# Kernel tuning notes

Measured on AMD Instinct MI355X. Metric: run time of the kernel, lower is better.

The kernel has to match this reference:

```python
import jax, jax.numpy as jnp
import numpy as np

N = 50000   # nodes
DEG = 16    # avg degree
E = N * DEG # edges
D = 64      # 2*vl, vl=32
EPS = 1e-12 # F.normalize eps


def setup_inputs() -> dict:
    key = jax.random.key(0)
    k1, k2, k3, k4 = jax.random.split(key, 4)
    ft_lv0 = jax.random.normal(k1, (N, D), dtype=jnp.float32)
    # fc weights: Linear(4*vl, 2*vl, bias=False) -> shape [2*vl, 4*vl] = [64, 128]
    W1 = jax.random.normal(k2, (D, 2 * D), dtype=jnp.float32) * 0.05
    W2 = jax.random.normal(k3, (D, 2 * D), dtype=jnp.float32) * 0.05
    # edge list: tgt[e] gathers ft[nbr[e]] and sums into node tgt[e]
    nbr = jax.random.randint(k4, (E,), 0, N, dtype=jnp.int32)
    tgt = jnp.repeat(jnp.arange(N, dtype=jnp.int32), DEG)  # sorted segment ids
    return {"ft_lv0": ft_lv0, "W1": W1, "W2": W2, "nbr": nbr, "tgt": tgt}


def _gcn_layer(ft, W, nbr, tgt, n_nodes):
    # sum-pool neighbor features: pool[n] = sum_{m in adj(n)} ft[m]
    pool = jax.ops.segment_sum(ft[nbr], tgt, num_segments=n_nodes)  # [N, D]
    # concat(node + pool, node * pool); pool==0 for isolated nodes reproduces
    # the original else-branch cat(node, zeros) exactly.
    z = jnp.concatenate([ft + pool, ft * pool], axis=-1)  # [N, 2D]
    return jax.nn.relu(z @ W.T)  # [N, D]


def reference(ft_lv0, W1, W2, nbr, tgt):
    n_nodes = ft_lv0.shape[0]
    ft_lv1 = _gcn_layer(ft_lv0, W1, nbr, tgt, n_nodes)
    ft_lv2 = _gcn_layer(ft_lv1, W2, nbr, tgt, n_nodes)
    # F.normalize(z, dim=-1): z / max(||z||_2, eps)
    norm = jnp.linalg.norm(ft_lv2, axis=-1, keepdims=True)
    return ft_lv2 / jnp.maximum(norm, EPS)
```

## Files before the change

### kernel.cpp

```cpp
#include <hip/hip_runtime.h>
#include <hip/hip_bf16.h>


#define N_NODES 50000
#define DEG 16
#define DIM 64
#define NTILES 3125

typedef __attribute__((ext_vector_type(8))) short short8;
typedef __attribute__((ext_vector_type(8))) unsigned short ushort8;
typedef __attribute__((ext_vector_type(4))) float f32x4;

__device__ __forceinline__ unsigned short f2b(float f) {
  unsigned int u = __float_as_uint(f);
  u = (u + 0x7FFFu + ((u >> 16) & 1u)) >> 16;
  return (unsigned short)u;
}
#define LOF(u) __uint_as_float((u) << 16)
#define HIF(u) __uint_as_float((u) & 0xFFFF0000u)

__global__ void cast_bf16(const float* __restrict__ in, unsigned short* __restrict__ out, int n4) {
  const int i = blockIdx.x * 256 + threadIdx.x;
  if (i < n4) {
    const float4 v = reinterpret_cast<const float4*>(in)[i];
    ushort4 o4;
    o4.x = f2b(v.x); o4.y = f2b(v.y); o4.z = f2b(v.z); o4.w = f2b(v.w);
    reinterpret_cast<ushort4*>(out)[i] = o4;
  }
}

__global__ void prep_w(const float* __restrict__ W1, const float* __restrict__ W2,
                       unsigned short* __restrict__ Wb) {
  const int task = blockIdx.x * 256 + threadIdx.x;
  if (task >= 2048) return;
  const int which = task >> 10;
  const int f = (task >> 6) & 15;
  const int l = task & 63;
  const int ct = f >> 2, ks = f & 3;
  const int wn = l & 15, wg = l >> 4;
  const float* W = which ? W2 : W1;
  const float* wp = W + (ct * 16 + wn) * 128 + ks * 32 + wg * 8;
  const float4 w0 = *(const float4*)wp;
  const float4 w1 = *(const float4*)(wp + 4);
  ushort8 o;
  o[0] = f2b(w0.x); o[1] = f2b(w0.y); o[2] = f2b(w0.z); o[3] = f2b(w0.w);
  o[4] = f2b(w1.x); o[5] = f2b(w1.y); o[6] = f2b(w1.z); o[7] = f2b(w1.w);
  *(ushort8*)(Wb + ((size_t)(which * 16 + f) * 64 + l) * 8) = o;
}

#define GATHER_AND_STAGE_V3()                                                  \
  _Pragma("unroll 2")                                                          \
  for (int p = 0; p < 4; ++p) {                                                \
    const int pp = sub * 4 + p;                                                \
    const int rA = (base + 2 * pp) * DEG;                                      \
    const int4 ia0 = *(const int4*)(nbr + rA);                                 \
    const int4 ia1 = *(const int4*)(nbr + rA + 4);                             \
    const int4 ia2 = *(const int4*)(nbr + rA + 8);                             \
    const int4 ia3 = *(const int4*)(nbr + rA + 12);                            \
    const int4 ib0 = *(const int4*)(nbr + rA + 16);                            \
    const int4 ib1 = *(const int4*)(nbr + rA + 20);                            \
    const int4 ib2 = *(const int4*)(nbr + rA + 24);                            \
    const int4 ib3 = *(const int4*)(nbr + rA + 28);                            \
    const unsigned int un  = ftp[(base + 2 * pp + half) * 32 + c];             \
    const unsigned int v0  = ftp[(half ? ib0.x : ia0.x) * 32 + c];             \
    const unsigned int v1  = ftp[(half ? ib0.y : ia0.y) * 32 + c];             \
    const unsigned int v2  = ftp[(half ? ib0.z : ia0.z) * 32 + c];             \
    const unsigned int v3  = ftp[(half ? ib0.w : ia0.w) * 32 + c];             \
    const unsigned int v4  = ftp[(half ? ib1.x : ia1.x) * 32 + c];             \
    const unsigned int v5  = ftp[(half ? ib1.y : ia1.y) * 32 + c];             \
    const unsigned int v6  = ftp[(half ? ib1.z : ia1.z) * 32 + c];             \
    const unsigned int v7  = ftp[(half ? ib1.w : ia1.w) * 32 + c];             \
    const unsigned int v8  = ftp[(half ? ib2.x : ia2.x) * 32 + c];             \
    const unsigned int v9  = ftp[(half ? ib2.y : ia2.y) * 32 + c];             \
    const unsigned int v10 = ftp[(half ? ib2.z : ia2.z) * 32 + c];             \
    const unsigned int v11 = ftp[(half ? ib2.w : ia2.w) * 32 + c];             \
    const unsigned int v12 = ftp[(half ? ib3.x : ia3.x) * 32 + c];             \
    const unsigned int v13 = ftp[(half ? ib3.y : ia3.y) * 32 + c];             \
    const unsigned int v14 = ftp[(half ? ib3.z : ia3.z) * 32 + c];             \
    const unsigned int v15 = ftp[(half ? ib3.w : ia3.w) * 32 + c];             \
    const float plo = (((LOF(v0) + LOF(v1)) + (LOF(v2) + LOF(v3))) +           \
                       ((LOF(v4) + LOF(v5)) + (LOF(v6) + LOF(v7)))) +          \
                      (((LOF(v8) + LOF(v9)) + (LOF(v10) + LOF(v11))) +         \
                       ((LOF(v12) + LOF(v13)) + (LOF(v14) + LOF(v15))));       \
    const float phi = (((HIF(v0) + HIF(v1)) + (HIF(v2) + HIF(v3))) +           \
                       ((HIF(v4) + HIF(v5)) + (HIF(v6) + HIF(v7)))) +          \
                      (((HIF(v8) + HIF(v9)) + (HIF(v10) + HIF(v11))) +         \
                       ((HIF(v12) + HIF(v13)) + (HIF(v14) + HIF(v15))));       \
    const float nlo = LOF(un), nhi = HIF(un);                                  \
    const float z1lo = nlo + plo, z1hi = nhi + phi;                            \
    const float z2lo = nlo * plo, z2hi = nhi * phi;                            \
    unsigned int z1p, z2p;                                                     \
    asm("v_cvt_pk_bf16_f32 %0, %1, %2" : "=v"(z1p) : "v"(z1lo), "v"(z1hi));    \
    asm("v_cvt_pk_bf16_f32 %0, %1, %2" : "=v"(z2p) : "v"(z2lo), "v"(z2hi));    \
    const int r = 2 * pp + half;                                               \
    const int cs = c ^ ((r & 7) << 2);                                         \
    Azs[r * 64 + cs] = z1p;                                                    \
    Azs[r * 64 + 32 + cs] = z2p;                                               \
  }

#define PRELOAD_W()                                                            \
  short8 Bf[4][4];                                                             \
  {                                                                            \
    const short8* wf = (const short8*)Wb;                                      \
    _Pragma("unroll")                                                          \
    for (int f = 0; f < 16; ++f) Bf[f >> 2][f & 3] = wf[f * 64 + lane];        \
  }

#define MFMA_ACCUM()                                                           \
  f32x4 ac0 = {0.f, 0.f, 0.f, 0.f}, ac1 = ac0, ac2 = ac0, ac3 = ac0;          \
  {                                                                            \
    const int arow = lane & 15, agrp = lane >> 4;                              \
    const int axor = (arow & 7) << 2;                                          \
    _Pragma("unroll")                                                          \
    for (int ks = 0; ks < 4; ++ks) {                                           \
      const short8 a =                                                         \
          *(const short8*)&Azs[arow * 64 + ((ks * 16 + agrp * 4) ^ axor)];     \
      ac0 = __builtin_amdgcn_mfma_f32_16x16x32_bf16(a, Bf[0][ks], ac0, 0, 0, 0);\
      ac1 = __builtin_amdgcn_mfma_f32_16x16x32_bf16(a, Bf[1][ks], ac1, 0, 0, 0);\
      ac2 = __builtin_amdgcn_mfma_f32_16x16x32_bf16(a, Bf[2][ks], ac2, 0, 0, 0);\
      ac3 = __builtin_amdgcn_mfma_f32_16x16x32_bf16(a, Bf[3][ks], ac3, 0, 0, 0);\
    }                                                                          \
  }

__global__ __launch_bounds__(256, 4)
void gcn_mfma1(const unsigned short* __restrict__ ftb,
               const unsigned short* __restrict__ Wb,
               const int* __restrict__ nbr,
               unsigned short* __restrict__ outb) {
  __shared__ unsigned int Az[2][1024];
  const int tid = threadIdx.x;
  const int lane = tid & 63, wid = tid >> 6;
  const int tl = wid >> 1, sub = wid & 1;
  const int t = __builtin_amdgcn_readfirstlane(blockIdx.x * 2 + tl);
  const bool active = (t < NTILES);
  const int base = t * 16;
  const int half = lane >> 5, c = lane & 31;
  const unsigned int* ftp = (const unsigned int*)ftb;
  unsigned int* Azs = &Az[tl][0];

  if (active) { GATHER_AND_STAGE_V3(); }
  PRELOAD_W();
  __syncthreads();
  MFMA_ACCUM();
  __syncthreads();

  if (active) {
    unsigned short* sh = (unsigned short*)Azs;
    const int colf = lane & 15, rgrp = lane >> 4;
    if ((rgrp >> 1) == sub) {
#define STG1(AC, CT)                                                           \
      _Pragma("unroll")                                                        \
      for (int rr = 0; rr < 4; ++rr)                                           \
        sh[(rgrp * 4 + rr) * 64 + (((CT)*16 + colf) ^ (rgrp << 4))] =          \
            f2b(fmaxf(AC[rr], 0.f));
      STG1(ac0, 0) STG1(ac1, 1) STG1(ac2, 2) STG1(ac3, 3)
#undef STG1
    }
    const int row = sub * 8 + (lane >> 3), b = lane & 7;
    const int rg = row >> 2;
    const ushort8 d = *(const ushort8*)&sh[row * 64 + ((b ^ (rg << 1)) << 3)];
    *(ushort8*)(outb + (size_t)(base + row) * 64 + b * 8) = d;
  }
}

__global__ __launch_bounds__(256, 4)
void gcn_mfma2(const unsigned short* __restrict__ ftb,
               const unsigned short* __restrict__ Wb,
               const int* __restrict__ nbr,
               float* __restrict__ out) {
  __shared__ unsigned int Az[2][1024];
  const int tid = threadIdx.x;
  const int lane = tid & 63, wid = tid >> 6;
  const int tl = wid >> 1, sub = wid & 1;
  const int t = __builtin_amdgcn_readfirstlane(blockIdx.x * 2 + tl);
  const bool active = (t < NTILES);
  const int base = t * 16;
  const int half = lane >> 5, c = lane & 31;
  const unsigned int* ftp = (const unsigned int*)ftb;
  unsigned int* Azs = &Az[tl][0];

  if (active) { GATHER_AND_STAGE_V3(); }
  PRELOAD_W();
  __syncthreads();
  MFMA_ACCUM();
  __syncthreads();

  if (active) {
    float v0[4], v1[4], v2[4], v3[4];
#pragma unroll
    for (int rr = 0; rr < 4; ++rr) {
      v0[rr] = fmaxf(ac0[rr], 0.f);
      v1[rr] = fmaxf(ac1[rr], 0.f);
      v2[rr] = fmaxf(ac2[rr], 0.f);
      v3[rr] = fmaxf(ac3[rr], 0.f);
    }
    float s0 = v0[0]*v0[0] + v1[0]*v1[0] + v2[0]*v2[0] + v3[0]*v3[0];
    float s1 = v0[1]*v0[1] + v1[1]*v1[1] + v2[1]*v2[1] + v3[1]*v3[1];
    float s2 = v0[2]*v0[2] + v1[2]*v1[2] + v2[2]*v2[2] + v3[2]*v3[2];
    float s3 = v0[3]*v0[3] + v1[3]*v1[3] + v2[3]*v2[3] + v3[3]*v3[3];
#pragma unroll
    for (int w = 1; w < 16; w <<= 1) {
      s0 += __shfl_xor(s0, w, 64);
      s1 += __shfl_xor(s1, w, 64);
      s2 += __shfl_xor(s2, w, 64);
      s3 += __shfl_xor(s3, w, 64);
    }
    const float kk[4] = {1.f / fmaxf(sqrtf(s0), 1e-12f),
                         1.f / fmaxf(sqrtf(s1), 1e-12f),
                         1.f / fmaxf(sqrtf(s2), 1e-12f),
                         1.f / fmaxf(sqrtf(s3), 1e-12f)};

    float* shf = (float*)Azs;
    const int colf = lane & 15, rgrp = lane >> 4;
    if ((rgrp >> 1) == sub) {
#define STG2(VA, CT)                                                           \
      _Pragma("unroll")                                                        \
      for (int rr = 0; rr < 4; ++rr)                                           \
        shf[(rgrp * 4 + rr) * 64 + (((CT)*16 + colf) ^ (rgrp << 4))] =         \
            VA[rr] * kk[rr];
      STG2(v0, 0) STG2(v1, 1) STG2(v2, 2) STG2(v3, 3)
#undef STG2
    }
    const int row = sub * 8 + (lane >> 3);
    const int rg = row >> 2;
    float* op = out + (size_t)(base + row) * 64;
#pragma unroll
    for (int e = 0; e < 2; ++e) {
      const int c4 = (lane & 7) * 2 + e;
      *(float4*)(op + c4 * 4) =
          *(const float4*)&shf[row * 64 + ((c4 ^ (rg << 2)) << 2)];
    }
  }
}

extern "C" void kernel_launch(void* const* d_in, const int* in_sizes, int n_in,
                              void* d_out, int out_size, void* d_ws, size_t ws_size,
                              hipStream_t stream) {
  const float* ft0;
  const float* W1;
  const float* W2;
  const int*   nbr;
  if (in_sizes[0] == N_NODES * DIM) {
    ft0 = (const float*)d_in[0];
    W1  = (const float*)d_in[1];
    W2  = (const float*)d_in[2];
    nbr = (const int*)d_in[3];
  } else {
    W1  = (const float*)d_in[0];
    W2  = (const float*)d_in[1];
    ft0 = (const float*)d_in[2];
    nbr = (const int*)d_in[3];
  }

  unsigned short* ftb0 = (unsigned short*)d_ws;
  unsigned short* ft1b = ftb0 + (size_t)N_NODES * DIM;
  unsigned short* Wb   = ft1b + (size_t)N_NODES * DIM;
  float* out = (float*)d_out;

  const int n4 = (N_NODES * DIM) / 4;
  cast_bf16<<<dim3((n4 + 255) / 256), dim3(256), 0, stream>>>(ft0, ftb0, n4);
  prep_w<<<dim3(8), dim3(256), 0, stream>>>(W1, W2, Wb);

  const int nblk = (NTILES + 1) / 2;
  gcn_mfma1<<<dim3(nblk), dim3(256), 0, stream>>>(ftb0, Wb, nbr, ft1b);
  gcn_mfma2<<<dim3(nblk), dim3(256), 0, stream>>>(ft1b, Wb + 8192, nbr, out);
}
```

Measured before the change: 114.2 us.

## Stage weights in LDS, split MFMA columns across waves, merge prep kernels

Merges the feature cast and weight-prep kernels into one launch. In both GCN layers the weight fragments now go into shared memory instead of being preloaded into 16 short8 registers per lane. Each of the two waves per tile computes only half of the output columns instead of all 64 redundantly. The second layer combines per-wave partial row norms through a small shared array with one extra barrier. This cuts register pressure and duplicate MFMA work, at the cost of more LDS traffic and a larger LDS footprint per block.

```diff
diff --git a/kernel.cpp b/kernel.cpp
--- a/kernel.cpp
+++ b/kernel.cpp
@@ -6,10 +6,12 @@
 #define DEG 16
 #define DIM 64
 #define NTILES 3125
+#define CAST_BLOCKS 3125
 
 typedef __attribute__((ext_vector_type(8))) short short8;
 typedef __attribute__((ext_vector_type(8))) unsigned short ushort8;
 typedef __attribute__((ext_vector_type(4))) float f32x4;
+typedef __attribute__((ext_vector_type(4))) unsigned int uint4v;
 
 __device__ __forceinline__ unsigned short f2b(float f) {
   unsigned int u = __float_as_uint(f);
@@ -19,36 +21,35 @@
 #define LOF(u) __uint_as_float((u) << 16)
 #define HIF(u) __uint_as_float((u) & 0xFFFF0000u)
 
-__global__ void cast_bf16(const float* __restrict__ in, unsigned short* __restrict__ out, int n4) {
-  const int i = blockIdx.x * 256 + threadIdx.x;
-  if (i < n4) {
-    const float4 v = reinterpret_cast<const float4*>(in)[i];
+__global__ void prep(const float* __restrict__ ft0,
+                     const float* __restrict__ W1, const float* __restrict__ W2,
+                     unsigned short* __restrict__ ftb, unsigned short* __restrict__ Wb) {
+  const int b = blockIdx.x;
+  if (b < CAST_BLOCKS) {
+    const int i = b * 256 + threadIdx.x;
+    const float4 v = reinterpret_cast<const float4*>(ft0)[i];
     ushort4 o4;
     o4.x = f2b(v.x); o4.y = f2b(v.y); o4.z = f2b(v.z); o4.w = f2b(v.w);
-    reinterpret_cast<ushort4*>(out)[i] = o4;
-  }
-}
-
-__global__ void prep_w(const float* __restrict__ W1, const float* __restrict__ W2,
-                       unsigned short* __restrict__ Wb) {
-  const int task = blockIdx.x * 256 + threadIdx.x;
-  if (task >= 2048) return;
-  const int which = task >> 10;
-  const int f = (task >> 6) & 15;
-  const int l = task & 63;
-  const int ct = f >> 2, ks = f & 3;
-  const int wn = l & 15, wg = l >> 4;
-  const float* W = which ? W2 : W1;
-  const float* wp = W + (ct * 16 + wn) * 128 + ks * 32 + wg * 8;
-  const float4 w0 = *(const float4*)wp;
-  const float4 w1 = *(const float4*)(wp + 4);
-  ushort8 o;
-  o[0] = f2b(w0.x); o[1] = f2b(w0.y); o[2] = f2b(w0.z); o[3] = f2b(w0.w);
-  o[4] = f2b(w1.x); o[5] = f2b(w1.y); o[6] = f2b(w1.z); o[7] = f2b(w1.w);
-  *(ushort8*)(Wb + ((size_t)(which * 16 + f) * 64 + l) * 8) = o;
-}
-
-#define GATHER_AND_STAGE_V3()                                                  \
+    reinterpret_cast<ushort4*>(ftb)[i] = o4;
+  } else {
+    const int task = (b - CAST_BLOCKS) * 256 + threadIdx.x;
+    if (task >= 2048) return;
+    const int which = task >> 10;
+    const int f = (task >> 6) & 15;
+    const int l = task & 63;
+    const int ct = f >> 2, ks = f & 3;
+    const float* W = which ? W2 : W1;
+    const float* wp = W + (ct * 16 + (l & 15)) * 128 + ks * 32 + (l >> 4) * 8;
+    const float4 w0 = *(const float4*)wp;
+    const float4 w1 = *(const float4*)(wp + 4);
+    ushort8 o;
+    o[0] = f2b(w0.x); o[1] = f2b(w0.y); o[2] = f2b(w0.z); o[3] = f2b(w0.w);
+    o[4] = f2b(w1.x); o[5] = f2b(w1.y); o[6] = f2b(w1.z); o[7] = f2b(w1.w);
+    *(ushort8*)(Wb + ((size_t)(which * 16 + f) * 64 + l) * 8) = o;
+  }
+}
+
+#define GATHER_AND_STAGE()                                                     \
   _Pragma("unroll 2")                                                          \
   for (int p = 0; p < 4; ++p) {                                                \
     const int pp = sub * 4 + p;                                                \
@@ -98,27 +99,28 @@
     Azs[r * 64 + 32 + cs] = z2p;                                               \
   }
 
-#define PRELOAD_W()                                                            \
-  short8 Bf[4][4];                                                             \
+#define LOAD_WLDS()                                                            \
   {                                                                            \
-    const short8* wf = (const short8*)Wb;                                      \
+    const uint4v* src = (const uint4v*)Wb;                                     \
+    uint4v* dst = (uint4v*)Wlds;                                               \
     _Pragma("unroll")                                                          \
-    for (int f = 0; f < 16; ++f) Bf[f >> 2][f & 3] = wf[f * 64 + lane];        \
+    for (int i = 0; i < 4; ++i) dst[i * 256 + tid] = src[i * 256 + tid];       \
   }
 
 #define MFMA_ACCUM()                                                           \
-  f32x4 ac0 = {0.f, 0.f, 0.f, 0.f}, ac1 = ac0, ac2 = ac0, ac3 = ac0;          \
+  f32x4 ac0 = {0.f, 0.f, 0.f, 0.f}, ac1 = ac0;                                \
   {                                                                            \
     const int arow = lane & 15, agrp = lane >> 4;                              \
     const int axor = (arow & 7) << 2;                                          \
+    const short8* wlds8 = (const short8*)Wlds;                                 \
     _Pragma("unroll")                                                          \
     for (int ks = 0; ks < 4; ++ks) {                                           \
       const short8 a =                                                         \
           *(const short8*)&Azs[arow * 64 + ((ks * 16 + agrp * 4) ^ axor)];     \
-      ac0 = __builtin_amdgcn_mfma_f32_16x16x32_bf16(a, Bf[0][ks], ac0, 0, 0, 0);\
-      ac1 = __builtin_amdgcn_mfma_f32_16x16x32_bf16(a, Bf[1][ks], ac1, 0, 0, 0);\
-      ac2 = __builtin_amdgcn_mfma_f32_16x16x32_bf16(a, Bf[2][ks], ac2, 0, 0, 0);\
-      ac3 = __builtin_amdgcn_mfma_f32_16x16x32_bf16(a, Bf[3][ks], ac3, 0, 0, 0);\
+      const short8 b0 = wlds8[((sub * 2 + 0) * 4 + ks) * 64 + lane];           \
+      const short8 b1 = wlds8[((sub * 2 + 1) * 4 + ks) * 64 + lane];           \
+      ac0 = __builtin_amdgcn_mfma_f32_16x16x32_bf16(a, b0, ac0, 0, 0, 0);      \
+      ac1 = __builtin_amdgcn_mfma_f32_16x16x32_bf16(a, b1, ac1, 0, 0, 0);      \
     }                                                                          \
   }
 
@@ -127,6 +129,7 @@
                const unsigned short* __restrict__ Wb,
                const int* __restrict__ nbr,
                unsigned short* __restrict__ outb) {
+  __shared__ unsigned int Wlds[4096];
   __shared__ unsigned int Az[2][1024];
   const int tid = threadIdx.x;
   const int lane = tid & 63, wid = tid >> 6;
@@ -138,28 +141,23 @@
   const unsigned int* ftp = (const unsigned int*)ftb;
   unsigned int* Azs = &Az[tl][0];
 
-  if (active) { GATHER_AND_STAGE_V3(); }
-  PRELOAD_W();
+  LOAD_WLDS();
+  if (active) { GATHER_AND_STAGE(); }
   __syncthreads();
   MFMA_ACCUM();
   __syncthreads();
 
   if (active) {
-    unsigned short* sh = (unsigned short*)Azs;
+    unsigned short* slab = (unsigned short*)Azs + sub * 512;
     const int colf = lane & 15, rgrp = lane >> 4;
-    if ((rgrp >> 1) == sub) {
-#define STG1(AC, CT)                                                           \
-      _Pragma("unroll")                                                        \
-      for (int rr = 0; rr < 4; ++rr)                                           \
-        sh[(rgrp * 4 + rr) * 64 + (((CT)*16 + colf) ^ (rgrp << 4))] =          \
-            f2b(fmaxf(AC[rr], 0.f));
-      STG1(ac0, 0) STG1(ac1, 1) STG1(ac2, 2) STG1(ac3, 3)
-#undef STG1
-    }
-    const int row = sub * 8 + (lane >> 3), b = lane & 7;
-    const int rg = row >> 2;
-    const ushort8 d = *(const ushort8*)&sh[row * 64 + ((b ^ (rg << 1)) << 3)];
-    *(ushort8*)(outb + (size_t)(base + row) * 64 + b * 8) = d;
+#pragma unroll
+    for (int rr = 0; rr < 4; ++rr) {
+      slab[(rgrp * 4 + rr) * 32 + colf]      = f2b(fmaxf(ac0[rr], 0.f));
+      slab[(rgrp * 4 + rr) * 32 + 16 + colf] = f2b(fmaxf(ac1[rr], 0.f));
+    }
+    const int row = lane >> 2, chunk = lane & 3;
+    const ushort8 d = *(const ushort8*)&slab[row * 32 + chunk * 8];
+    *(ushort8*)(outb + (size_t)(base + row) * 64 + sub * 32 + chunk * 8) = d;
   }
 }
 
@@ -168,7 +166,9 @@
                const unsigned short* __restrict__ Wb,
                const int* __restrict__ nbr,
                float* __restrict__ out) {
+  __shared__ unsigned int Wlds[4096];
   __shared__ unsigned int Az[2][1024];
+  __shared__ float sP[2][2][16];
   const int tid = threadIdx.x;
   const int lane = tid & 63, wid = tid >> 6;
   const int tl = wid >> 1, sub = wid & 1;
@@ -179,25 +179,24 @@
   const unsigned int* ftp = (const unsigned int*)ftb;
   unsigned int* Azs = &Az[tl][0];
 
-  if (active) { GATHER_AND_STAGE_V3(); }
-  PRELOAD_W();
+  LOAD_WLDS();
+  if (active) { GATHER_AND_STAGE(); }
   __syncthreads();
   MFMA_ACCUM();
-  __syncthreads();
-
+
+  float v0[4], v1[4];
+  const int colf = lane & 15, rgrp = lane >> 4;
   if (active) {
-    float v0[4], v1[4], v2[4], v3[4];
+    float s0, s1, s2, s3;
 #pragma unroll
     for (int rr = 0; rr < 4; ++rr) {
       v0[rr] = fmaxf(ac0[rr], 0.f);
       v1[rr] = fmaxf(ac1[rr], 0.f);
-      v2[rr] = fmaxf(ac2[rr], 0.f);
-      v3[rr] = fmaxf(ac3[rr], 0.f);
-    }
-    float s0 = v0[0]*v0[0] + v1[0]*v1[0] + v2[0]*v2[0] + v3[0]*v3[0];
-    float s1 = v0[1]*v0[1] + v1[1]*v1[1] + v2[1]*v2[1] + v3[1]*v3[1];
-    float s2 = v0[2]*v0[2] + v1[2]*v1[2] + v2[2]*v2[2] + v3[2]*v3[2];
-    float s3 = v0[3]*v0[3] + v1[3]*v1[3] + v2[3]*v2[3] + v3[3]*v3[3];
+    }
+    s0 = v0[0] * v0[0] + v1[0] * v1[0];
+    s1 = v0[1] * v0[1] + v1[1] * v1[1];
+    s2 = v0[2] * v0[2] + v1[2] * v1[2];
+    s3 = v0[3] * v0[3] + v1[3] * v1[3];
 #pragma unroll
     for (int w = 1; w < 16; w <<= 1) {
       s0 += __shfl_xor(s0, w, 64);
@@ -205,31 +204,32 @@
       s2 += __shfl_xor(s2, w, 64);
       s3 += __shfl_xor(s3, w, 64);
     }
-    const float kk[4] = {1.f / fmaxf(sqrtf(s0), 1e-12f),
-                         1.f / fmaxf(sqrtf(s1), 1e-12f),
-                         1.f / fmaxf(sqrtf(s2), 1e-12f),
-                         1.f / fmaxf(sqrtf(s3), 1e-12f)};
-
-    float* shf = (float*)Azs;
-    const int colf = lane & 15, rgrp = lane >> 4;
-    if ((rgrp >> 1) == sub) {
-#define STG2(VA, CT)                                                           \
-      _Pragma("unroll")                                                        \
-      for (int rr = 0; rr < 4; ++rr)                                           \
-        shf[(rgrp * 4 + rr) * 64 + (((CT)*16 + colf) ^ (rgrp << 4))] =         \
-            VA[rr] * kk[rr];
-      STG2(v0, 0) STG2(v1, 1) STG2(v2, 2) STG2(v3, 3)
-#undef STG2
-    }
-    const int row = sub * 8 + (lane >> 3);
-    const int rg = row >> 2;
-    float* op = out + (size_t)(base + row) * 64;
-#pragma unroll
-    for (int e = 0; e < 2; ++e) {
-      const int c4 = (lane & 7) * 2 + e;
-      *(float4*)(op + c4 * 4) =
-          *(const float4*)&shf[row * 64 + ((c4 ^ (rg << 2)) << 2)];
-    }
+    if (colf == 0) {
+      sP[tl][sub][rgrp * 4 + 0] = s0;
+      sP[tl][sub][rgrp * 4 + 1] = s1;
+      sP[tl][sub][rgrp * 4 + 2] = s2;
+      sP[tl][sub][rgrp * 4 + 3] = s3;
+    }
+  }
+  __syncthreads();
+
+  if (active) {
+    float kk[4];
+#pragma unroll
+    for (int rr = 0; rr < 4; ++rr) {
+      const float s = sP[tl][0][rgrp * 4 + rr] + sP[tl][1][rgrp * 4 + rr];
+      kk[rr] = 1.f / fmaxf(sqrtf(s), 1e-12f);
+    }
+    float* slab = (float*)Azs + sub * 512;
+#pragma unroll
+    for (int rr = 0; rr < 4; ++rr) {
+      slab[(rgrp * 4 + rr) * 32 + colf]      = v0[rr] * kk[rr];
+      slab[(rgrp * 4 + rr) * 32 + 16 + colf] = v1[rr] * kk[rr];
+    }
+    const int row = lane >> 2, chunk = lane & 3;
+    float* op = out + (size_t)(base + row) * 64 + sub * 32 + chunk * 4;
+    *(float4*)op        = *(const float4*)&slab[row * 32 + chunk * 4];
+    *(float4*)(op + 16) = *(const float4*)&slab[row * 32 + chunk * 4 + 16];
   }
 }
 
@@ -257,9 +257,7 @@
   unsigned short* Wb   = ft1b + (size_t)N_NODES * DIM;
   float* out = (float*)d_out;
 
-  const int n4 = (N_NODES * DIM) / 4;
-  cast_bf16<<<dim3((n4 + 255) / 256), dim3(256), 0, stream>>>(ft0, ftb0, n4);
-  prep_w<<<dim3(8), dim3(256), 0, stream>>>(W1, W2, Wb);
+  prep<<<dim3(CAST_BLOCKS + 8), dim3(256), 0, stream>>>(ft0, W1, W2, ftb0, Wb);
 
   const int nblk = (NTILES + 1) / 2;
   gcn_mfma1<<<dim3(nblk), dim3(256), 0, stream>>>(ftb0, Wb, nbr, ft1b);
```

Measured after the change: 108.1 us. 1.06x faster.
